# Kernel tuning notes

Measured on AMD Instinct MI355X. Metric: run time of the kernel, lower is better.

## Reference

```python
import jax, jax.numpy as jnp
import numpy as np

EMBED = 1024
HEADS = 16
HEAD_DIM = EMBED // HEADS
MLP_DIM = 4096
EPS = 1e-5


def setup_inputs() -> dict:
    key = jax.random.key(0)
    ks = jax.random.split(key, 12)
    s = lambda d: 1.0 / np.sqrt(d)
    return {
        "x": jax.random.normal(ks[0], (8, 1024, EMBED), dtype=jnp.float32),
        "ln1_g": jnp.ones((EMBED,), jnp.float32),
        "ln1_b": jnp.zeros((EMBED,), jnp.float32),
        "w_qkv": jax.random.normal(ks[1], (EMBED, 3 * EMBED), jnp.float32) * s(EMBED),
        "b_qkv": jnp.zeros((3 * EMBED,), jnp.float32),
        "w_proj": jax.random.normal(ks[2], (EMBED, EMBED), jnp.float32) * s(EMBED),
        "b_proj": jnp.zeros((EMBED,), jnp.float32),
        "ln2_g": jnp.ones((EMBED,), jnp.float32),
        "ln2_b": jnp.zeros((EMBED,), jnp.float32),
        "w_fc1": jax.random.normal(ks[3], (EMBED, MLP_DIM), jnp.float32) * s(EMBED),
        "b_fc1": jnp.zeros((MLP_DIM,), jnp.float32),
        "w_fc2": jax.random.normal(ks[4], (MLP_DIM, EMBED), jnp.float32) * s(MLP_DIM),
        "b_fc2": jnp.zeros((EMBED,), jnp.float32),
    }


def _layernorm(x, g, b):
    mu = jnp.mean(x, axis=-1, keepdims=True)
    var = jnp.mean(jnp.square(x - mu), axis=-1, keepdims=True)
    return (x - mu) * jax.lax.rsqrt(var + EPS) * g + b


def reference(x, ln1_g, ln1_b, w_qkv, b_qkv, w_proj, b_proj,
              ln2_g, ln2_b, w_fc1, b_fc1, w_fc2, b_fc2):
    B, N, D = x.shape
    scale = HEAD_DIM ** -0.5

    # --- attention branch ---
    h = _layernorm(x, ln1_g, ln1_b)
    qkv = h @ w_qkv + b_qkv                       # [B,N,3D]
    qkv = qkv.reshape(B, N, 3, HEADS, HEAD_DIM)
    q, k, v = jnp.moveaxis(qkv, 2, 0)             # each [B,N,H,hd]
    attn = jnp.einsum('bqhd,bkhd->bhqk', q, k) * scale
    attn = jax.nn.softmax(attn, axis=-1)
    out = jnp.einsum('bhqk,bkhd->bqhd', attn, v).reshape(B, N, D)
    x = x + (out @ w_proj + b_proj)

    # --- MLP branch ---
    h = _layernorm(x, ln2_g, ln2_b)
    h = jax.nn.gelu(h @ w_fc1 + b_fc1, approximate=False)
    x = x + (h @ w_fc2 + b_fc2)
    return x
```

## Files before the change

kernel.cpp:

```cpp
#include <hip/hip_runtime.h>
#include <cstdint>


typedef unsigned short u16;
typedef short short8 __attribute__((ext_vector_type(8)));
typedef float floatx4 __attribute__((ext_vector_type(4)));

#define GLB(p) ((const __attribute__((address_space(1))) void*)(p))
#define LDSP(p) ((__attribute__((address_space(3))) void*)(p))

__device__ __forceinline__ u16 f2bf(float f) {
    uint32_t u = __float_as_uint(f);
    u += 0x7fffu + ((u >> 16) & 1u);
    return (u16)(u >> 16);
}
__device__ __forceinline__ uint32_t pack2(float a, float b) {
    return (uint32_t)f2bf(a) | ((uint32_t)f2bf(b) << 16);
}
__device__ __forceinline__ float fast_gelu(float v) {
    float u = v * (0.7978845608f + 0.0356774081f * v * v);
    float e = __expf(2.0f * u);
    float th = 1.0f - 2.0f * __builtin_amdgcn_rcpf(e + 1.0f);
    return 0.5f * v * (1.0f + th);
}

__global__ __launch_bounds__(256) void transpose_cast_kernel(
    const float* __restrict__ W, u16* __restrict__ Wt, int K, int N)
{
    __shared__ float tile[32][33];
    int n0 = blockIdx.x * 32, k0 = blockIdx.y * 32;
    int tx = threadIdx.x, ty = threadIdx.y;
    #pragma unroll
    for (int i = 0; i < 4; ++i)
        tile[ty + i * 8][tx] = W[(size_t)(k0 + ty + i * 8) * N + n0 + tx];
    __syncthreads();
    #pragma unroll
    for (int i = 0; i < 4; ++i)
        Wt[(size_t)(n0 + ty + i * 8) * K + k0 + tx] = f2bf(tile[tx][ty + i * 8]);
}

__global__ __launch_bounds__(256) void ln_kernel(
    const float* __restrict__ x, const float* __restrict__ gw,
    const float* __restrict__ bw, u16* __restrict__ out)
{
    const int row = blockIdx.x, tid = threadIdx.x;
    float4 v = ((const float4*)(x + (size_t)row * 1024))[tid];
    float s  = v.x + v.y + v.z + v.w;
    float ss = v.x * v.x + v.y * v.y + v.z * v.z + v.w * v.w;
    #pragma unroll
    for (int off = 32; off > 0; off >>= 1) {
        s  += __shfl_down(s, off);
        ss += __shfl_down(ss, off);
    }
    __shared__ float red[8];
    if ((tid & 63) == 0) { red[tid >> 6] = s; red[4 + (tid >> 6)] = ss; }
    __syncthreads();
    float S  = red[0] + red[1] + red[2] + red[3];
    float SS = red[4] + red[5] + red[6] + red[7];
    float mu  = S * (1.0f / 1024.0f);
    float var = SS * (1.0f / 1024.0f) - mu * mu;
    float rs  = rsqrtf(var + 1e-5f);
    float4 g4 = ((const float4*)gw)[tid];
    float4 b4 = ((const float4*)bw)[tid];
    u16* o = out + (size_t)row * 1024 + tid * 4;
    o[0] = f2bf((v.x - mu) * rs * g4.x + b4.x);
    o[1] = f2bf((v.y - mu) * rs * g4.y + b4.y);
    o[2] = f2bf((v.z - mu) * rs * g4.z + b4.z);
    o[3] = f2bf((v.w - mu) * rs * g4.w + b4.w);
}

#define MODE_BF16      0
#define MODE_BF16_GELU 1
#define MODE_F32_RES   2
#define MODE_QKV       3

template<int MODE>
__global__ __launch_bounds__(256) void gemm_bt_kernel(
    const u16* __restrict__ A, const u16* __restrict__ Bt,
    const float* __restrict__ bias, const float* __restrict__ res,
    void* __restrict__ outv, u16* __restrict__ vt, int M, int N, int K)
{
    __shared__ __attribute__((aligned(16))) u16 As[128 * 64];
    __shared__ __attribute__((aligned(16))) u16 Bs[128 * 64];
    const int tid = threadIdx.x;
    const int wave = tid >> 6, lane = tid & 63;
    const int lg = lane >> 4, lc = lane & 15;
    const int m0 = blockIdx.y * 128, n0 = blockIdx.x * 128;
    const int wr = wave >> 1, wc = wave & 1;

    floatx4 acc[4][4];
    #pragma unroll
    for (int i = 0; i < 4; ++i)
        #pragma unroll
        for (int j = 0; j < 4; ++j) acc[i][j] = floatx4{0.f, 0.f, 0.f, 0.f};

    const int srow = lane >> 3;
    const int schunk = (lane & 7) ^ srow;
    const u16* Ag = A  + (size_t)(m0 + wave * 32 + srow) * K + schunk * 8;
    const u16* Bg = Bt + (size_t)(n0 + wave * 32 + srow) * K + schunk * 8;
    u16* Asw = &As[wave * 4 * 512];
    u16* Bsw = &Bs[wave * 4 * 512];

    const int kiters = K >> 6;
    for (int kt = 0; kt < kiters; ++kt) {
        #pragma unroll
        for (int j = 0; j < 4; ++j) {
            __builtin_amdgcn_global_load_lds(GLB(Ag + (size_t)j * 8 * K), LDSP(Asw + j * 512), 16, 0, 0);
            __builtin_amdgcn_global_load_lds(GLB(Bg + (size_t)j * 8 * K), LDSP(Bsw + j * 512), 16, 0, 0);
        }
        Ag += 64; Bg += 64;
        __syncthreads();
        #pragma unroll
        for (int ks = 0; ks < 2; ++ks) {
            short8 fa[4], fb[4];
            #pragma unroll
            for (int mt = 0; mt < 4; ++mt)
                fa[mt] = *(const short8*)&As[(wr * 64 + mt * 16 + lc) * 64 +
                                             (((ks * 4 + lg) ^ (lc & 7)) * 8)];
            #pragma unroll
            for (int nt = 0; nt < 4; ++nt)
                fb[nt] = *(const short8*)&Bs[(wc * 64 + nt * 16 + lc) * 64 +
                                             (((ks * 4 + lg) ^ (lc & 7)) * 8)];
            #pragma unroll
            for (int mt = 0; mt < 4; ++mt)
                #pragma unroll
                for (int nt = 0; nt < 4; ++nt)
                    acc[mt][nt] = __builtin_amdgcn_mfma_f32_16x16x32_bf16(fa[mt], fb[nt], acc[mt][nt], 0, 0, 0);
        }
        __syncthreads();
    }

    if (MODE == MODE_QKV && n0 >= 2048) {
        #pragma unroll
        for (int mt = 0; mt < 4; ++mt) {
            #pragma unroll
            for (int nt = 0; nt < 4; ++nt) {
                const int col = n0 + wc * 64 + nt * 16 + lc;
                const float bv = bias[col];
                const int hd = col - 2048;
                const int rowbase = m0 + wr * 64 + mt * 16 + lg * 4;
                const int b = rowbase >> 10, token = rowbase & 1023;
                float v0 = acc[mt][nt][0] + bv, v1 = acc[mt][nt][1] + bv;
                float v2 = acc[mt][nt][2] + bv, v3 = acc[mt][nt][3] + bv;
                uint2 pk = {pack2(v0, v1), pack2(v2, v3)};
                *(uint2*)&vt[((size_t)b * 1024 + hd) * 1024 + token] = pk;
            }
        }
        return;
    }
    #pragma unroll
    for (int mt = 0; mt < 4; ++mt) {
        #pragma unroll
        for (int nt = 0; nt < 4; ++nt) {
            const int col = n0 + wc * 64 + nt * 16 + lc;
            const float bv = bias[col];
            #pragma unroll
            for (int r = 0; r < 4; ++r) {
                const int row = m0 + wr * 64 + mt * 16 + lg * 4 + r;
                float v = acc[mt][nt][r] + bv;
                if (MODE == MODE_BF16 || MODE == MODE_QKV) {
                    ((u16*)outv)[(size_t)row * N + col] = f2bf(v);
                } else if (MODE == MODE_BF16_GELU) {
                    ((u16*)outv)[(size_t)row * N + col] = f2bf(fast_gelu(v));
                } else {
                    ((float*)outv)[(size_t)row * N + col] = v + res[(size_t)row * N + col];
                }
            }
        }
    }
}

__global__ __launch_bounds__(256) void attn_kernel(
    const u16* __restrict__ qkv, const u16* __restrict__ vtg, u16* __restrict__ out)
{
    const int bid = blockIdx.x;
    const int g = ((bid >> 7) << 3) | (bid & 7);
    const int qt = (bid >> 3) & 15;
    const int h = g & 15, b = g >> 4;
    const int tid = threadIdx.x, wave = tid >> 6, lane = tid & 63;
    const int lg = lane >> 4, lc = lane & 15;

    __shared__ __attribute__((aligned(16))) u16 Qs[64 * 64];
    __shared__ __attribute__((aligned(16))) u16 Ks[64 * 64];
    __shared__ __attribute__((aligned(16))) u16 Vts[64 * 64];
    __shared__ __attribute__((aligned(16))) u16 Ps[64 * 64];

    const int q0 = qt * 64;
    const size_t hb = ((size_t)b * 1024) * 3072 + h * 64;
    const u16* vhead = vtg + ((size_t)b * 1024 + h * 64) * 1024;
    const int srow = lane >> 3;
    const int schunk = (lane & 7) ^ srow;

    {
        const u16* Qg = qkv + hb + (size_t)(q0 + wave * 16 + srow) * 3072 + schunk * 8;
        u16* Qw = &Qs[wave * 1024];
        __builtin_amdgcn_global_load_lds(GLB(Qg), LDSP(Qw), 16, 0, 0);
        __builtin_amdgcn_global_load_lds(GLB(Qg + (size_t)8 * 3072), LDSP(Qw + 512), 16, 0, 0);
    }
    __syncthreads();
    short8 aq[2];
    aq[0] = *(const short8*)&Qs[(wave * 16 + lc) * 64 + (((0 + lg) ^ (lc & 7)) * 8)];
    aq[1] = *(const short8*)&Qs[(wave * 16 + lc) * 64 + (((4 + lg) ^ (lc & 7)) * 8)];

    floatx4 o[4];
    #pragma unroll
    for (int dt = 0; dt < 4; ++dt) o[dt] = floatx4{0.f, 0.f, 0.f, 0.f};
    float mprev = -INFINITY, lsum = 0.f;
    const float sc = 0.125f;

    for (int kt = 0; kt < 16; ++kt) {
        __syncthreads();
        {
            const u16* Kg = qkv + hb + 1024 +
                (size_t)(kt * 64 + wave * 16 + srow) * 3072 + schunk * 8;
            u16* Kw = &Ks[wave * 1024];
            __builtin_amdgcn_global_load_lds(GLB(Kg), LDSP(Kw), 16, 0, 0);
            __builtin_amdgcn_global_load_lds(GLB(Kg + (size_t)8 * 3072), LDSP(Kw + 512), 16, 0, 0);
        }
        {
            const u16* Vg = vhead + (size_t)(wave * 16 + srow) * 1024 + kt * 64 + schunk * 8;
            u16* Vw = &Vts[wave * 1024];
            __builtin_amdgcn_global_load_lds(GLB(Vg), LDSP(Vw), 16, 0, 0);
            __builtin_amdgcn_global_load_lds(GLB(Vg + (size_t)8 * 1024), LDSP(Vw + 512), 16, 0, 0);
        }
        __syncthreads();

        floatx4 st[4];
        #pragma unroll
        for (int nt = 0; nt < 4; ++nt) st[nt] = floatx4{0.f, 0.f, 0.f, 0.f};
        #pragma unroll
        for (int ks = 0; ks < 2; ++ks)
            #pragma unroll
            for (int nt = 0; nt < 4; ++nt) {
                short8 fk = *(const short8*)&Ks[(nt * 16 + lc) * 64 +
                                                (((ks * 4 + lg) ^ (lc & 7)) * 8)];
                st[nt] = __builtin_amdgcn_mfma_f32_16x16x32_bf16(fk, aq[ks], st[nt], 0, 0, 0);
            }

        float m = st[0][0];
        #pragma unroll
        for (int nt = 0; nt < 4; ++nt)
            #pragma unroll
            for (int r = 0; r < 4; ++r) m = fmaxf(m, st[nt][r]);
        m = fmaxf(m, __shfl_xor(m, 16));
        m = fmaxf(m, __shfl_xor(m, 32));
        float mn = fmaxf(mprev, m * sc);
        float aexp = __expf(mprev - mn);
        mprev = mn;

        const int q = wave * 16 + lc;
        float rs = 0.f;
        #pragma unroll
        for (int nt = 0; nt < 4; ++nt) {
            float p0 = __expf(st[nt][0] * sc - mn);
            float p1 = __expf(st[nt][1] * sc - mn);
            float p2 = __expf(st[nt][2] * sc - mn);
            float p3 = __expf(st[nt][3] * sc - mn);
            rs += (p0 + p1) + (p2 + p3);
            const int c16 = nt * 2 + (lg >> 1);
            uint2 pk = {pack2(p0, p1), pack2(p2, p3)};
            *(uint2*)&Ps[q * 64 + ((c16 ^ (lc & 7)) * 8) + (lg & 1) * 4] = pk;
        }
        rs += __shfl_xor(rs, 16);
        rs += __shfl_xor(rs, 32);
        lsum = lsum * aexp + rs;
        #pragma unroll
        for (int dt = 0; dt < 4; ++dt)
            #pragma unroll
            for (int r = 0; r < 4; ++r) o[dt][r] *= aexp;

        #pragma unroll
        for (int ks = 0; ks < 2; ++ks) {
            short8 fp = *(const short8*)&Ps[q * 64 + (((ks * 4 + lg) ^ (lc & 7)) * 8)];
            #pragma unroll
            for (int dt = 0; dt < 4; ++dt) {
                short8 fv = *(const short8*)&Vts[(dt * 16 + lc) * 64 +
                                                 (((ks * 4 + lg) ^ (lc & 7)) * 8)];
                o[dt] = __builtin_amdgcn_mfma_f32_16x16x32_bf16(fv, fp, o[dt], 0, 0, 0);
            }
        }
    }

    const float rl = 1.0f / lsum;
    const int q = q0 + wave * 16 + lc;
    #pragma unroll
    for (int dt = 0; dt < 4; ++dt) {
        uint2 pk = {pack2(o[dt][0] * rl, o[dt][1] * rl),
                    pack2(o[dt][2] * rl, o[dt][3] * rl)};
        *(uint2*)&out[((size_t)b * 1024 + q) * 1024 + h * 64 + dt * 16 + lg * 4] = pk;
    }
}

extern "C" void kernel_launch(void* const* d_in, const int* in_sizes, int n_in,
                              void* d_out, int out_size, void* d_ws, size_t ws_size,
                              hipStream_t stream)
{
    const float* x      = (const float*)d_in[0];
    const float* ln1_g  = (const float*)d_in[1];
    const float* ln1_b  = (const float*)d_in[2];
    const float* w_qkv  = (const float*)d_in[3];
    const float* b_qkv  = (const float*)d_in[4];
    const float* w_proj = (const float*)d_in[5];
    const float* b_proj = (const float*)d_in[6];
    const float* ln2_g  = (const float*)d_in[7];
    const float* ln2_b  = (const float*)d_in[8];
    const float* w_fc1  = (const float*)d_in[9];
    const float* b_fc1  = (const float*)d_in[10];
    const float* w_fc2  = (const float*)d_in[11];
    const float* b_fc2  = (const float*)d_in[12];
    float* outp = (float*)d_out;

    char* ws = (char*)d_ws;
    size_t off = 0;
    auto alloc = [&](size_t bytes) { void* p = ws + off; off += (bytes + 255) & ~(size_t)255; return p; };
    u16*  wqkvT  = (u16*)alloc((size_t)3072 * 1024 * 2);
    u16*  wprojT = (u16*)alloc((size_t)1024 * 1024 * 2);
    u16*  wfc1T  = (u16*)alloc((size_t)4096 * 1024 * 2);
    u16*  wfc2T  = (u16*)alloc((size_t)1024 * 4096 * 2);
    u16*  hbuf   = (u16*)alloc((size_t)8192 * 1024 * 2);
    u16*  big    = (u16*)alloc((size_t)8192 * 4096 * 2);
    u16*  vtbuf  = (u16*)alloc((size_t)8 * 1024 * 1024 * 2);
    u16*  attno  = (u16*)alloc((size_t)8192 * 1024 * 2);
    float* x2    = (float*)alloc((size_t)8192 * 1024 * 4);

    dim3 tb(32, 8);
    transpose_cast_kernel<<<dim3(3072 / 32, 1024 / 32), tb, 0, stream>>>(w_qkv,  wqkvT,  1024, 3072);
    transpose_cast_kernel<<<dim3(1024 / 32, 1024 / 32), tb, 0, stream>>>(w_proj, wprojT, 1024, 1024);
    transpose_cast_kernel<<<dim3(4096 / 32, 1024 / 32), tb, 0, stream>>>(w_fc1,  wfc1T,  1024, 4096);
    transpose_cast_kernel<<<dim3(1024 / 32, 4096 / 32), tb, 0, stream>>>(w_fc2,  wfc2T,  4096, 1024);

    ln_kernel<<<8192, 256, 0, stream>>>(x, ln1_g, ln1_b, hbuf);
    gemm_bt_kernel<MODE_QKV><<<dim3(3072 / 128, 8192 / 128), 256, 0, stream>>>(
        hbuf, wqkvT, b_qkv, nullptr, big, vtbuf, 8192, 3072, 1024);
    attn_kernel<<<2048, 256, 0, stream>>>(big, vtbuf, attno);
    gemm_bt_kernel<MODE_F32_RES><<<dim3(1024 / 128, 8192 / 128), 256, 0, stream>>>(
        attno, wprojT, b_proj, x, x2, nullptr, 8192, 1024, 1024);
    ln_kernel<<<8192, 256, 0, stream>>>(x2, ln2_g, ln2_b, hbuf);
    gemm_bt_kernel<MODE_BF16_GELU><<<dim3(4096 / 128, 8192 / 128), 256, 0, stream>>>(
        hbuf, wfc1T, b_fc1, nullptr, big, nullptr, 8192, 4096, 1024);
    gemm_bt_kernel<MODE_F32_RES><<<dim3(1024 / 128, 8192 / 128), 256, 0, stream>>>(
        big, wfc2T, b_fc2, x2, outp, nullptr, 8192, 1024, 4096);
}
```

Before: 510.5 us.

## Double-buffer B tiles in LDS and stream A fragments directly into registers

```diff
diff --git a/kernel.cpp b/kernel.cpp
--- a/kernel.cpp
+++ b/kernel.cpp
@@ -75,13 +75,12 @@
 #define MODE_QKV       3
 
 template<int MODE>
-__global__ __launch_bounds__(256) void gemm_bt_kernel(
+__global__ __launch_bounds__(256, 3) void gemm_bt_kernel(
     const u16* __restrict__ A, const u16* __restrict__ Bt,
     const float* __restrict__ bias, const float* __restrict__ res,
     void* __restrict__ outv, u16* __restrict__ vt, int M, int N, int K)
 {
-    __shared__ __attribute__((aligned(16))) u16 As[128 * 64];
-    __shared__ __attribute__((aligned(16))) u16 Bs[128 * 64];
+    __shared__ __attribute__((aligned(16))) u16 Bs[2][128 * 64];
     const int tid = threadIdx.x;
     const int wave = tid >> 6, lane = tid & 63;
     const int lg = lane >> 4, lc = lane & 15;
@@ -96,38 +95,53 @@
 
     const int srow = lane >> 3;
     const int schunk = (lane & 7) ^ srow;
-    const u16* Ag = A  + (size_t)(m0 + wave * 32 + srow) * K + schunk * 8;
-    const u16* Bg = Bt + (size_t)(n0 + wave * 32 + srow) * K + schunk * 8;
-    u16* Asw = &As[wave * 4 * 512];
-    u16* Bsw = &Bs[wave * 4 * 512];
-
-    const int kiters = K >> 6;
-    for (int kt = 0; kt < kiters; ++kt) {
-        #pragma unroll
-        for (int j = 0; j < 4; ++j) {
-            __builtin_amdgcn_global_load_lds(GLB(Ag + (size_t)j * 8 * K), LDSP(Asw + j * 512), 16, 0, 0);
-            __builtin_amdgcn_global_load_lds(GLB(Bg + (size_t)j * 8 * K), LDSP(Bsw + j * 512), 16, 0, 0);
-        }
-        Ag += 64; Bg += 64;
-        __syncthreads();
+    const u16* Bk = Bt + (size_t)(n0 + wave * 32 + srow) * K + schunk * 8;
+    const u16* Ak = A  + (size_t)(m0 + wr * 64 + lc) * K + lg * 8;
+    u16* Bsw0 = &Bs[0][wave * 2048];
+    u16* Bsw1 = &Bs[1][wave * 2048];
+
+    short8 fa0[4][2], fa1[4][2];
+
+    auto issueB = [&](u16* dst, const u16* src) {
+        #pragma unroll
+        for (int j = 0; j < 4; ++j)
+            __builtin_amdgcn_global_load_lds(GLB(src + (size_t)j * 8 * K), LDSP(dst + j * 512), 16, 0, 0);
+    };
+    auto loadA = [&](short8 (&fa)[4][2], const u16* p) {
+        #pragma unroll
+        for (int mt = 0; mt < 4; ++mt)
+            #pragma unroll
+            for (int ks = 0; ks < 2; ++ks)
+                fa[mt][ks] = *(const short8*)(p + (size_t)mt * 16 * K + ks * 32);
+    };
+    auto compute = [&](short8 (&fa)[4][2], const u16* bs) {
         #pragma unroll
         for (int ks = 0; ks < 2; ++ks) {
-            short8 fa[4], fb[4];
-            #pragma unroll
-            for (int mt = 0; mt < 4; ++mt)
-                fa[mt] = *(const short8*)&As[(wr * 64 + mt * 16 + lc) * 64 +
-                                             (((ks * 4 + lg) ^ (lc & 7)) * 8)];
+            short8 fb[4];
             #pragma unroll
             for (int nt = 0; nt < 4; ++nt)
-                fb[nt] = *(const short8*)&Bs[(wc * 64 + nt * 16 + lc) * 64 +
+                fb[nt] = *(const short8*)&bs[(wc * 64 + nt * 16 + lc) * 64 +
                                              (((ks * 4 + lg) ^ (lc & 7)) * 8)];
             #pragma unroll
             for (int mt = 0; mt < 4; ++mt)
                 #pragma unroll
                 for (int nt = 0; nt < 4; ++nt)
-                    acc[mt][nt] = __builtin_amdgcn_mfma_f32_16x16x32_bf16(fa[mt], fb[nt], acc[mt][nt], 0, 0, 0);
-        }
+                    acc[mt][nt] = __builtin_amdgcn_mfma_f32_16x16x32_bf16(fa[mt][ks], fb[nt], acc[mt][nt], 0, 0, 0);
+        }
+    };
+
+    const int kiters = K >> 6;
+    issueB(Bsw0, Bk);
+    loadA(fa0, Ak);
+    __syncthreads();
+    for (int kt = 0; kt < kiters; kt += 2) {
+        if (kt + 1 < kiters) { issueB(Bsw1, Bk + 64); loadA(fa1, Ak + 64); }
+        compute(fa0, Bs[0]);
         __syncthreads();
+        if (kt + 2 < kiters) { issueB(Bsw0, Bk + 128); loadA(fa0, Ak + 128); }
+        compute(fa1, Bs[1]);
+        __syncthreads();
+        Ak += 128; Bk += 128;
     }
 
     if (MODE == MODE_QKV && n0 >= 2048) {
```

New measurement: 1.058 ms. 107% more time.
